# Kernel optimization log

Hardware: AMD Instinct MI355X
Metric: run time of the kernel (lower is better)

Reference implementation:

```python
import jax, jax.numpy as jnp
import numpy as np

L = 4


def make_coord(h, w):
    # pixel-center coords in [-1,1], shape (h*w, 2), dim order (y, x)
    ys = -1.0 + 1.0 / h + (2.0 / h) * jnp.arange(h, dtype=jnp.float32)
    xs = -1.0 + 1.0 / w + (2.0 / w) * jnp.arange(w, dtype=jnp.float32)
    gy, gx = jnp.meshgrid(ys, xs, indexing='ij')
    return jnp.stack([gy, gx], axis=-1).reshape(-1, 2)


def bilinear_sample(feat, gx, gy):
    # feat: (B,C,H,W); gx,gy in [-1,1], shape (B,N); align_corners=True
    B, C, H, W = feat.shape
    ix = (gx + 1.0) * 0.5 * (W - 1)
    iy = (gy + 1.0) * 0.5 * (H - 1)
    x0f = jnp.floor(ix)
    y0f = jnp.floor(iy)
    x0 = jnp.clip(x0f.astype(jnp.int32), 0, W - 1)
    x1 = jnp.clip(x0 + 1, 0, W - 1)
    y0 = jnp.clip(y0f.astype(jnp.int32), 0, H - 1)
    y1 = jnp.clip(y0 + 1, 0, H - 1)
    wx1 = ix - x0f
    wx0 = 1.0 - wx1
    wy1 = iy - y0f
    wy0 = 1.0 - wy1
    featf = feat.reshape(B, C, H * W)

    def g(yi, xi):
        idx = yi * W + xi  # (B,N)
        return jnp.take_along_axis(featf, idx[:, None, :], axis=2)  # (B,C,N)

    out = (g(y0, x0) * (wy0 * wx0)[:, None, :] + g(y0, x1) * (wy0 * wx1)[:, None, :]
           + g(y1, x0) * (wy1 * wx0)[:, None, :] + g(y1, x1) * (wy1 * wx1)[:, None, :])
    return out.transpose(0, 2, 1)  # (B,N,C)


def pos_enc(x):
    # x: (B,N,2) -> (B,N,4L); per dim: [sin_0..sin_{L-1}, cos_0..cos_{L-1}]
    freq = (2.0 ** jnp.arange(L, dtype=jnp.float32)) * np.pi
    spec = x[..., None] * freq  # (B,N,2,L)
    enc = jnp.concatenate([jnp.sin(spec), jnp.cos(spec)], axis=-1)  # (B,N,2,2L)
    return enc.reshape(*x.shape[:-1], 4 * L)


def mlp(x, w0, b0, w1, b1, w2, b2, w3, b3):
    h = jax.nn.relu(x @ w0 + b0)
    h = jax.nn.relu(h @ w1 + b1)
    h = jax.nn.relu(h @ w2 + b2)
    return h @ w3 + b3


def setup_inputs() -> dict:
    key = jax.random.key(0)
    ks = jax.random.split(key, 8)
    B, C, H, W = 4, 64, 128, 128
    hid, out_dim = 256, 3
    in_dim = C + 2 + 4 * L + 2  # 84
    s = 0.05
    return {
        'inp': jax.random.normal(ks[0], (B, C, H, W), jnp.float32),
        'w0': jax.random.normal(ks[1], (in_dim, hid), jnp.float32) * s,
        'b0': jnp.zeros((hid,), jnp.float32),
        'w1': jax.random.normal(ks[2], (hid, hid), jnp.float32) * s,
        'b1': jnp.zeros((hid,), jnp.float32),
        'w2': jax.random.normal(ks[3], (hid, hid), jnp.float32) * s,
        'b2': jnp.zeros((hid,), jnp.float32),
        'w3': jax.random.normal(ks[4], (hid, out_dim), jnp.float32) * s,
        'b3': jnp.zeros((out_dim,), jnp.float32),
        'scale': 2,
    }


def reference(inp, w0, b0, w1, b1, w2, b2, w3, b3, scale):
    B, C, H, W = inp.shape
    th, tw = int(round(H * scale)), int(round(W * scale))
    N = th * tw
    coord = jnp.broadcast_to(make_coord(th, tw)[None], (B, N, 2))
    # cell = (2/th, 2/tw); rel_cell = cell * (H, W)
    rel_cell = jnp.broadcast_to(
        jnp.array([2.0 / th * H, 2.0 / tw * W], jnp.float32), (B, N, 2))
    # feature-pixel coordinate map, appended as extra channels so one gather serves both
    fc = make_coord(H, W).reshape(H, W, 2).transpose(2, 0, 1)  # (2,H,W)
    aug = jnp.concatenate([inp, jnp.broadcast_to(fc[None], (B, 2, H, W))], axis=1)

    pe = pos_enc(coord)  # same for all 4 ensemble branches
    hw_scale = jnp.array([H, W], jnp.float32)
    rx, ry = 1.0 / H, 1.0 / W
    eps = 1e-6

    preds, areas = [], []
    for vx in (-1, 1):
        for vy in (-1, 1):
            c0 = jnp.clip(coord[..., 0] + vx * rx + eps, -1 + 1e-6, 1 - 1e-6)
            c1 = jnp.clip(coord[..., 1] + vy * ry + eps, -1 + 1e-6, 1 - 1e-6)
            # grid_sample uses (x, y) = flipped coord -> gx=c1, gy=c0
            q = bilinear_sample(aug, c1, c0)  # (B,N,C+2)
            q_feat, q_coord = q[..., :C], q[..., C:]
            rel = (coord - q_coord) * hw_scale  # (B,N,2)
            x = jnp.concatenate([q_feat, rel, pe, rel_cell], axis=-1)
            preds.append(mlp(x, w0, b0, w1, b1, w2, b2, w3, b3))
            areas.append(jnp.abs(rel[..., 0] * rel[..., 1]) + 1e-9)

    areas = [areas[3], areas[2], areas[1], areas[0]]  # diagonal swap
    tot = areas[0] + areas[1] + areas[2] + areas[3]
    ret = sum(p * (a / tot)[..., None] for p, a in zip(preds, areas))  # (B,N,out)
    return ret.reshape(B, th, tw, -1).transpose(0, 3, 1, 2)  # (B,out,th,tw)
```

## Files before the change

kernel.cpp:

```cpp
#include <hip/hip_runtime.h>
#include <math.h>

#define NB 4
#define NH 128
#define NW 128
#define TH 256
#define TW 256
#define AST 264
#define K0 96
#define MROWS 256
#define PIXB 64

typedef _Float16 f16;
typedef f16  f16x8 __attribute__((ext_vector_type(8)));
typedef f16  f16x4v __attribute__((ext_vector_type(4)));
typedef float f32x4 __attribute__((ext_vector_type(4)));
typedef float f32x16 __attribute__((ext_vector_type(16)));

#define OFF_W1 24576
#define OFF_W2 (OFF_W1 + 65536)
#define OFF_W3 (OFF_W2 + 65536)
#define OFF_PE (OFF_W3 + 4096)
#define WS_W_ELEMS (OFF_PE + 4096)
#define FT_ELEMS (NB * NH * NW * 64)

__global__ void cvt_weights(const float* __restrict__ w0, const float* __restrict__ w1,
                            const float* __restrict__ w2, const float* __restrict__ w3,
                            f16* __restrict__ ws) {
  const int i = blockIdx.x * 256 + threadIdx.x;
  if (i < 24576) {
    const int n = i / 96, k = i - n * 96;
    ws[i] = (k < 84) ? (f16)w0[k * 256 + n] : (f16)0.f;
  } else if (i < OFF_W2) {
    const int j = i - OFF_W1; const int n = j >> 8, k = j & 255;
    ws[i] = (f16)w1[k * 256 + n];
  } else if (i < OFF_W3) {
    const int j = i - OFF_W2; const int n = j >> 8, k = j & 255;
    ws[i] = (f16)w2[k * 256 + n];
  } else if (i < OFF_PE) {
    const int j = i - OFF_W3; const int n = j >> 8, k = j & 255;
    ws[i] = (n < 3) ? (f16)w3[k * 3 + n] : (f16)0.f;
  } else if (i < WS_W_ELEMS) {
    const int j = i - OFF_PE;
    const int o = (j & 2047) >> 3, e = j & 7;
    const float c = (2.0f * o + 1.0f) / 256.0f - 1.0f;
    const float f = (float)(1 << (e & 3)) * (float)M_PI;
    ws[i] = (f16)((e < 4) ? sinf(c * f) : cosf(c * f));
  }
}

__global__ void transpose_feat(const float* __restrict__ feat, f16* __restrict__ ft) {
  __shared__ f16 tile[64][66];
  const int bid = blockIdx.x;
  const int xt = bid & 1, y = (bid >> 1) & 127, b = bid >> 8;
  const int x0 = xt * 64;
  {
    const int c4 = threadIdx.x >> 6, x = threadIdx.x & 63;
#pragma unroll
    for (int co = 0; co < 16; ++co) {
      const int c = co * 4 + c4;
      tile[x][c] = (f16)feat[((size_t)(b * 64 + c) * NH + y) * NW + x0 + x];
    }
  }
  __syncthreads();
  {
    const int x4 = threadIdx.x >> 6, c = threadIdx.x & 63;
#pragma unroll
    for (int xo = 0; xo < 16; ++xo) {
      const int x = xo * 4 + x4;
      ft[((size_t)(b * NH + y) * NW + x0 + x) * 64 + c] = tile[x][c];
    }
  }
}

template<int K>
__device__ __forceinline__ void dense_layer(const f16* __restrict__ Wt,
                                            const float* __restrict__ bias,
                                            f16* act, int wm, int wn, int l) {
  constexpr int NK = K / 16;
  const int lo = l & 31, hi = l >> 5;
  const f16* Abase = Wt + (size_t)(wn * 64 + lo) * K + hi * 8;
  const f16* Bbase = act + (wm * 128 + lo) * AST + hi * 8;

  f32x16 acc[2][4];
#pragma unroll
  for (int nt = 0; nt < 2; ++nt) {
    f32x16 ci;
#pragma unroll
    for (int g = 0; g < 4; ++g) {
      const float4 b4 = *(const float4*)(bias + wn * 64 + nt * 32 + 8 * g + 4 * hi);
      ci[4 * g + 0] = b4.x; ci[4 * g + 1] = b4.y; ci[4 * g + 2] = b4.z; ci[4 * g + 3] = b4.w;
    }
#pragma unroll
    for (int mt = 0; mt < 4; ++mt) acc[nt][mt] = ci;
  }

  f16x8 Ab[3][2], Bb[3][4];
#pragma unroll
  for (int p = 0; p < 2; ++p) {
#pragma unroll
    for (int nt = 0; nt < 2; ++nt) Ab[p][nt] = *(const f16x8*)(Abase + nt * 32 * K + p * 16);
#pragma unroll
    for (int mt = 0; mt < 4; ++mt) Bb[p][mt] = *(const f16x8*)(Bbase + mt * 32 * AST + p * 16);
  }

#pragma unroll
  for (int ks = 0; ks < NK; ++ks) {
    if (ks + 2 < NK) {
      const int d = (ks + 2) % 3;
#pragma unroll
      for (int nt = 0; nt < 2; ++nt) Ab[d][nt] = *(const f16x8*)(Abase + nt * 32 * K + (ks + 2) * 16);
#pragma unroll
      for (int mt = 0; mt < 4; ++mt) Bb[d][mt] = *(const f16x8*)(Bbase + mt * 32 * AST + (ks + 2) * 16);
    }
    const int c = ks % 3;
#pragma unroll
    for (int mt = 0; mt < 4; ++mt)
#pragma unroll
      for (int nt = 0; nt < 2; ++nt)
        acc[nt][mt] = __builtin_amdgcn_mfma_f32_32x32x16_f16(Ab[c][nt], Bb[c][mt], acc[nt][mt], 0, 0, 0);
  }

  __syncthreads();

#pragma unroll
  for (int nt = 0; nt < 2; ++nt)
#pragma unroll
    for (int mt = 0; mt < 4; ++mt)
#pragma unroll
      for (int g = 0; g < 4; ++g) {
        f16x4v o;
        o[0] = (f16)fmaxf(acc[nt][mt][4 * g + 0], 0.f);
        o[1] = (f16)fmaxf(acc[nt][mt][4 * g + 1], 0.f);
        o[2] = (f16)fmaxf(acc[nt][mt][4 * g + 2], 0.f);
        o[3] = (f16)fmaxf(acc[nt][mt][4 * g + 3], 0.f);
        *(f16x4v*)(act + (size_t)(wm * 128 + mt * 32 + lo) * AST +
                   wn * 64 + nt * 32 + 8 * g + 4 * hi) = o;
      }
}

template<bool USE_FT>
__global__ __launch_bounds__(512, 2) void inr2d_mfma(
    const float* __restrict__ feat, const f16* __restrict__ ft,
    const float* __restrict__ b0, const float* __restrict__ b1,
    const float* __restrict__ b2, const float* __restrict__ b3,
    const f16* __restrict__ ws, float* __restrict__ out)
{
  __shared__ f16 act[MROWS][AST];
  __shared__ float area_s[MROWS];
  __shared__ float pred_s[MROWS][4];

  const int t = threadIdx.x;
  const int blk = ((blockIdx.x & 7) << 9) | (blockIdx.x >> 3);

  {
    const int r = t >> 1, sub = t & 1;
    const int pix = r >> 2, e = r & 3;
    const int gp = blk * PIXB + pix;
    const int b = gp >> 16, rem = gp & 65535;
    const int oy = rem >> 8, ox = rem & 255;

    const float cy = (2.0f * oy + 1.0f) / (float)TH - 1.0f;
    const float cx = (2.0f * ox + 1.0f) / (float)TW - 1.0f;
    const float vx = (e & 2) ? 1.0f : -1.0f;
    const float vy = (e & 1) ? 1.0f : -1.0f;
    const float rr = 1.0f / (float)NH;

    float c0 = fminf(fmaxf(cy + vx * rr + 1e-6f, -1.0f + 1e-6f), 1.0f - 1e-6f);
    float c1 = fminf(fmaxf(cx + vy * rr + 1e-6f, -1.0f + 1e-6f), 1.0f - 1e-6f);

    const float ix = (c1 + 1.0f) * 0.5f * (float)(NW - 1);
    const float iy = (c0 + 1.0f) * 0.5f * (float)(NH - 1);
    const float x0f = floorf(ix), y0f = floorf(iy);
    int x0 = (int)x0f; x0 = max(0, min(x0, NW - 1));
    int x1 = min(x0 + 1, NW - 1);
    int y0 = (int)y0f; y0 = max(0, min(y0, NH - 1));
    int y1 = min(y0 + 1, NH - 1);
    const float wx1 = ix - x0f, wx0 = 1.0f - wx1;
    const float wy1 = iy - y0f, wy0 = 1.0f - wy1;
    const float w00 = wy0 * wx0, w01 = wy0 * wx1, w10 = wy1 * wx0, w11 = wy1 * wx1;

    if (USE_FT) {
      const f16* fb = ft + (size_t)b * (NH * NW * 64);
      const f16* r00 = fb + (size_t)(y0 * NW + x0) * 64 + sub * 32;
      const f16* r01 = fb + (size_t)(y0 * NW + x1) * 64 + sub * 32;
      const f16* r10 = fb + (size_t)(y1 * NW + x0) * 64 + sub * 32;
      const f16* r11 = fb + (size_t)(y1 * NW + x1) * 64 + sub * 32;
#pragma unroll
      for (int h = 0; h < 4; ++h) {
        const f16x8 a00 = *(const f16x8*)(r00 + h * 8);
        const f16x8 a01 = *(const f16x8*)(r01 + h * 8);
        const f16x8 a10 = *(const f16x8*)(r10 + h * 8);
        const f16x8 a11 = *(const f16x8*)(r11 + h * 8);
#pragma unroll
        for (int i = 0; i < 8; ++i) {
          const float v = w00 * (float)a00[i] + w01 * (float)a01[i] +
                          w10 * (float)a10[i] + w11 * (float)a11[i];
          act[r][sub * 32 + h * 8 + i] = (f16)v;
        }
      }
    } else {
      const float* fb = feat + (size_t)b * 64 * NH * NW;
      const int i00 = y0 * NW + x0, i01 = y0 * NW + x1;
      const int i10 = y1 * NW + x0, i11 = y1 * NW + x1;
#pragma unroll
      for (int i = 0; i < 32; ++i) {
        const int c = sub * 32 + i;
        const float* fc = fb + (size_t)c * (NH * NW);
        const float v = w00 * fc[i00] + w01 * fc[i01] + w10 * fc[i10] + w11 * fc[i11];
        act[r][c] = (f16)v;
      }
    }
    if (sub == 0) {
      const float qy = -1.0f + 1.0f / NH + (2.0f / NH) * (wy0 * (float)y0 + wy1 * (float)y1);
      const float qx = -1.0f + 1.0f / NW + (2.0f / NW) * (wx0 * (float)x0 + wx1 * (float)x1);
      const float rely = (cy - qy) * (float)NH;
      const float relx = (cx - qx) * (float)NW;
      act[r][64] = (f16)rely;
      act[r][65] = (f16)relx;
      if (USE_FT) {
        const f16* py = ws + OFF_PE + (size_t)oy * 8;
        const f16* px = ws + OFF_PE + 2048 + (size_t)ox * 8;
#pragma unroll
        for (int j = 0; j < 8; ++j) { act[r][66 + j] = py[j]; act[r][74 + j] = px[j]; }
      } else {
#pragma unroll
        for (int ll = 0; ll < 4; ++ll) {
          const float f = (float)(1 << ll) * (float)M_PI;
          act[r][66 + ll] = (f16)sinf(cy * f);
          act[r][70 + ll] = (f16)cosf(cy * f);
          act[r][74 + ll] = (f16)sinf(cx * f);
          act[r][78 + ll] = (f16)cosf(cx * f);
        }
      }
      act[r][82] = (f16)1.0f;
      act[r][83] = (f16)1.0f;
#pragma unroll
      for (int z = 84; z < K0; ++z) act[r][z] = (f16)0.f;
      area_s[r] = fabsf(rely * relx) + 1e-9f;
    }
  }
  __syncthreads();

  const int w = t >> 6, l = t & 63;
  const int wm = w >> 2, wn = w & 3;

  dense_layer<K0 >(ws,          b0, &act[0][0], wm, wn, l);
  __syncthreads();
  dense_layer<256>(ws + OFF_W1, b1, &act[0][0], wm, wn, l);
  __syncthreads();
  dense_layer<256>(ws + OFF_W2, b2, &act[0][0], wm, wn, l);
  __syncthreads();

  {
    const int nl = l & 15, kq = l >> 4;
    const f16* Abase = ws + OFF_W3 + nl * 256 + kq * 8;
#pragma unroll
    for (int p = 0; p < 2; ++p) {
      const f16* Bbase = &act[w * 32 + p * 16 + nl][0] + kq * 8;
      f32x4 acc = {0.f, 0.f, 0.f, 0.f};
#pragma unroll
      for (int ks = 0; ks < 8; ++ks) {
        f16x8 a = *(const f16x8*)(Abase + ks * 32);
        f16x8 b = *(const f16x8*)(Bbase + ks * 32);
        acc = __builtin_amdgcn_mfma_f32_16x16x32_f16(a, b, acc, 0, 0, 0);
      }
      if (l < 16) {
        float4 pr;
        pr.x = acc[0] + b3[0]; pr.y = acc[1] + b3[1]; pr.z = acc[2] + b3[2]; pr.w = 0.f;
        *(float4*)(&pred_s[w * 32 + p * 16 + l][0]) = pr;
      }
    }
  }
  __syncthreads();

  if (t < PIXB * 3) {
    const int pix = t / 3, o = t - pix * 3;
    const int gp = blk * PIXB + pix;
    const int b = gp >> 16, rem = gp & 65535;
    const int oy = rem >> 8, ox = rem & 255;
    const int r0 = pix * 4;
    const float a0 = area_s[r0], a1 = area_s[r0 + 1], a2 = area_s[r0 + 2], a3 = area_s[r0 + 3];
    const float tot = a0 + a1 + a2 + a3;
    const float v = pred_s[r0][o] * a3 + pred_s[r0 + 1][o] * a2 +
                    pred_s[r0 + 2][o] * a1 + pred_s[r0 + 3][o] * a0;
    out[(((size_t)b * 3 + o) << 16) + (oy << 8) + ox] = v / tot;
  }
}

extern "C" void kernel_launch(void* const* d_in, const int* in_sizes, int n_in,
                              void* d_out, int out_size, void* d_ws, size_t ws_size,
                              hipStream_t stream) {
  const float* feat = (const float*)d_in[0];
  const float* w0 = (const float*)d_in[1];
  const float* b0 = (const float*)d_in[2];
  const float* w1 = (const float*)d_in[3];
  const float* b1 = (const float*)d_in[4];
  const float* w2 = (const float*)d_in[5];
  const float* b2 = (const float*)d_in[6];
  const float* w3 = (const float*)d_in[7];
  const float* b3 = (const float*)d_in[8];
  float* out = (float*)d_out;
  f16* ws = (f16*)d_ws;

  cvt_weights<<<(WS_W_ELEMS + 255) / 256, 256, 0, stream>>>(w0, w1, w2, w3, ws);

  const int blocks = (NB * TH * TW) / PIXB;
  const bool use_ft = ws_size >= (size_t)(WS_W_ELEMS + FT_ELEMS) * sizeof(f16);
  if (use_ft) {
    f16* ft = ws + WS_W_ELEMS;
    transpose_feat<<<NB * NH * (NW / 64), 256, 0, stream>>>(feat, ft);
    inr2d_mfma<true><<<blocks, 512, 0, stream>>>(feat, ft, b0, b1, b2, b3, ws, out);
  } else {
    inr2d_mfma<false><<<blocks, 512, 0, stream>>>(feat, nullptr, b0, b1, b2, b3, ws, out);
  }
}
```

Before: 440.7 us.

## Stage MLP weight k-slices into LDS via direct global-to-LDS loads

Each dense layer now streams its weight k-slices into a triple-buffered LDS region with global_load_lds, so the whole block shares one copy instead of every wave loading its weight fragments from global or L2 separately. A barrier per k-step synchronises the buffer rotation, and MFMA issue is wrapped in s_setprio. The per-pixel prediction scratch is also shrunk to fp16 to free LDS for the weight buffers. This adds one barrier per k-step and slightly reduces output precision, and the extra LDS may affect the two-blocks-per-CU occupancy.

```diff
diff --git a/kernel.cpp b/kernel.cpp
--- a/kernel.cpp
+++ b/kernel.cpp
@@ -23,6 +23,12 @@
 #define OFF_PE (OFF_W3 + 4096)
 #define WS_W_ELEMS (OFF_PE + 4096)
 #define FT_ELEMS (NB * NH * NW * 64)
+
+__device__ __forceinline__ void gload_lds16(const f16* g, f16* l) {
+  __builtin_amdgcn_global_load_lds(
+      (const __attribute__((address_space(1))) void*)(g),
+      (__attribute__((address_space(3))) void*)(l), 16, 0, 0);
+}
 
 __global__ void cvt_weights(const float* __restrict__ w0, const float* __restrict__ w1,
                             const float* __restrict__ w2, const float* __restrict__ w3,
@@ -76,10 +82,13 @@
 template<int K>
 __device__ __forceinline__ void dense_layer(const f16* __restrict__ Wt,
                                             const float* __restrict__ bias,
-                                            f16* act, int wm, int wn, int l) {
+                                            f16* act, f16* wlds,
+                                            int wm, int wn, int l, int tid) {
   constexpr int NK = K / 16;
   const int lo = l & 31, hi = l >> 5;
-  const f16* Abase = Wt + (size_t)(wn * 64 + lo) * K + hi * 8;
+  const int sn = tid & 255, sh = tid >> 8;
+  const f16* src = Wt + (size_t)sn * K + sh * 8;
+  f16* wdst = wlds + (tid >> 6) * 512;
   const f16* Bbase = act + (wm * 128 + lo) * AST + hi * 8;
 
   f32x16 acc[2][4];
@@ -95,33 +104,38 @@
     for (int mt = 0; mt < 4; ++mt) acc[nt][mt] = ci;
   }
 
-  f16x8 Ab[3][2], Bb[3][4];
-#pragma unroll
-  for (int p = 0; p < 2; ++p) {
-#pragma unroll
-    for (int nt = 0; nt < 2; ++nt) Ab[p][nt] = *(const f16x8*)(Abase + nt * 32 * K + p * 16);
-#pragma unroll
-    for (int mt = 0; mt < 4; ++mt) Bb[p][mt] = *(const f16x8*)(Bbase + mt * 32 * AST + p * 16);
-  }
+  gload_lds16(src + 0 * 16, wdst + 0 * 4096);
+  gload_lds16(src + 1 * 16, wdst + 1 * 4096);
+  asm volatile("s_waitcnt vmcnt(1)" ::: "memory");
+  __builtin_amdgcn_s_barrier();
 
 #pragma unroll
   for (int ks = 0; ks < NK; ++ks) {
-    if (ks + 2 < NK) {
-      const int d = (ks + 2) % 3;
-#pragma unroll
-      for (int nt = 0; nt < 2; ++nt) Ab[d][nt] = *(const f16x8*)(Abase + nt * 32 * K + (ks + 2) * 16);
-#pragma unroll
-      for (int mt = 0; mt < 4; ++mt) Bb[d][mt] = *(const f16x8*)(Bbase + mt * 32 * AST + (ks + 2) * 16);
-    }
-    const int c = ks % 3;
-#pragma unroll
-    for (int mt = 0; mt < 4; ++mt)
-#pragma unroll
-      for (int nt = 0; nt < 2; ++nt)
-        acc[nt][mt] = __builtin_amdgcn_mfma_f32_32x32x16_f16(Ab[c][nt], Bb[c][mt], acc[nt][mt], 0, 0, 0);
-  }
-
-  __syncthreads();
+    if (ks + 2 < NK)
+      gload_lds16(src + (ks + 2) * 16, wdst + ((ks + 2) % 3) * 4096);
+
+    const f16* wb = wlds + (ks % 3) * 4096 + hi * 2048;
+    const f16x8 A0 = *(const f16x8*)(wb + (wn * 64 + 0 * 32 + lo) * 8);
+    const f16x8 A1 = *(const f16x8*)(wb + (wn * 64 + 1 * 32 + lo) * 8);
+    const f16x8 B0 = *(const f16x8*)(Bbase + 0 * 32 * AST + ks * 16);
+    const f16x8 B1 = *(const f16x8*)(Bbase + 1 * 32 * AST + ks * 16);
+    const f16x8 B2 = *(const f16x8*)(Bbase + 2 * 32 * AST + ks * 16);
+    const f16x8 B3 = *(const f16x8*)(Bbase + 3 * 32 * AST + ks * 16);
+
+    __builtin_amdgcn_s_setprio(1);
+    acc[0][0] = __builtin_amdgcn_mfma_f32_32x32x16_f16(A0, B0, acc[0][0], 0, 0, 0);
+    acc[0][1] = __builtin_amdgcn_mfma_f32_32x32x16_f16(A0, B1, acc[0][1], 0, 0, 0);
+    acc[0][2] = __builtin_amdgcn_mfma_f32_32x32x16_f16(A0, B2, acc[0][2], 0, 0, 0);
+    acc[0][3] = __builtin_amdgcn_mfma_f32_32x32x16_f16(A0, B3, acc[0][3], 0, 0, 0);
+    acc[1][0] = __builtin_amdgcn_mfma_f32_32x32x16_f16(A1, B0, acc[1][0], 0, 0, 0);
+    acc[1][1] = __builtin_amdgcn_mfma_f32_32x32x16_f16(A1, B1, acc[1][1], 0, 0, 0);
+    acc[1][2] = __builtin_amdgcn_mfma_f32_32x32x16_f16(A1, B2, acc[1][2], 0, 0, 0);
+    acc[1][3] = __builtin_amdgcn_mfma_f32_32x32x16_f16(A1, B3, acc[1][3], 0, 0, 0);
+    __builtin_amdgcn_s_setprio(0);
+
+    asm volatile("s_waitcnt vmcnt(1)" ::: "memory");
+    __builtin_amdgcn_s_barrier();
+  }
 
 #pragma unroll
   for (int nt = 0; nt < 2; ++nt)
@@ -147,8 +161,9 @@
     const f16* __restrict__ ws, float* __restrict__ out)
 {
   __shared__ f16 act[MROWS][AST];
+  __shared__ f16 wlds[3 * 4096];
   __shared__ float area_s[MROWS];
-  __shared__ float pred_s[MROWS][4];
+  __shared__ f16 pred_s[MROWS][4];
 
   const int t = threadIdx.x;
   const int blk = ((blockIdx.x & 7) << 9) | (blockIdx.x >> 3);
@@ -245,11 +260,11 @@
   const int w = t >> 6, l = t & 63;
   const int wm = w >> 2, wn = w & 3;
 
-  dense_layer<K0 >(ws,          b0, &act[0][0], wm, wn, l);
-  __syncthreads();
-  dense_layer<256>(ws + OFF_W1, b1, &act[0][0], wm, wn, l);
-  __syncthreads();
-  dense_layer<256>(ws + OFF_W2, b2, &act[0][0], wm, wn, l);
+  dense_layer<K0 >(ws,          b0, &act[0][0], wlds, wm, wn, l, t);
+  __syncthreads();
+  dense_layer<256>(ws + OFF_W1, b1, &act[0][0], wlds, wm, wn, l, t);
+  __syncthreads();
+  dense_layer<256>(ws + OFF_W2, b2, &act[0][0], wlds, wm, wn, l, t);
   __syncthreads();
 
   {
@@ -257,18 +272,19 @@
     const f16* Abase = ws + OFF_W3 + nl * 256 + kq * 8;
 #pragma unroll
     for (int p = 0; p < 2; ++p) {
-      const f16* Bbase = &act[w * 32 + p * 16 + nl][0] + kq * 8;
+      const f16* Bbase2 = &act[w * 32 + p * 16 + nl][0] + kq * 8;
       f32x4 acc = {0.f, 0.f, 0.f, 0.f};
 #pragma unroll
       for (int ks = 0; ks < 8; ++ks) {
         f16x8 a = *(const f16x8*)(Abase + ks * 32);
-        f16x8 b = *(const f16x8*)(Bbase + ks * 32);
+        f16x8 b = *(const f16x8*)(Bbase2 + ks * 32);
         acc = __builtin_amdgcn_mfma_f32_16x16x32_f16(a, b, acc, 0, 0, 0);
       }
       if (l < 16) {
-        float4 pr;
-        pr.x = acc[0] + b3[0]; pr.y = acc[1] + b3[1]; pr.z = acc[2] + b3[2]; pr.w = 0.f;
-        *(float4*)(&pred_s[w * 32 + p * 16 + l][0]) = pr;
+        f16x4v pr;
+        pr[0] = (f16)(acc[0] + b3[0]); pr[1] = (f16)(acc[1] + b3[1]);
+        pr[2] = (f16)(acc[2] + b3[2]); pr[3] = (f16)0.f;
+        *(f16x4v*)(&pred_s[w * 32 + p * 16 + l][0]) = pr;
       }
     }
   }
@@ -282,8 +298,8 @@
     const int r0 = pix * 4;
     const float a0 = area_s[r0], a1 = area_s[r0 + 1], a2 = area_s[r0 + 2], a3 = area_s[r0 + 3];
     const float tot = a0 + a1 + a2 + a3;
-    const float v = pred_s[r0][o] * a3 + pred_s[r0 + 1][o] * a2 +
-                    pred_s[r0 + 2][o] * a1 + pred_s[r0 + 3][o] * a0;
+    const float v = (float)pred_s[r0][o] * a3 + (float)pred_s[r0 + 1][o] * a2 +
+                    (float)pred_s[r0 + 2][o] * a1 + (float)pred_s[r0 + 3][o] * a0;
     out[(((size_t)b * 3 + o) << 16) + (oy << 8) + ox] = v / tot;
   }
 }
```

Result: no change. 437.5 us (-0.7%).
